# Optimization experiments

Hardware: AMD Instinct MI355X
Metric: run time of the kernel (lower is better)

Reference implementation:

```python
import jax, jax.numpy as jnp
import numpy as np

B, S, H = 2, 2048, 1024
G, HEADS = 4, 16
HPG = HEADS // G          # heads per group = 4
HD = H // HEADS           # head_dim = 64
DG = H // G               # per-group proj dim = 256
SCALE = 1.0 / np.sqrt(HD)


def setup_inputs() -> dict:
    key = jax.random.key(0)
    ks = jax.random.split(key, 6)
    w = 0.02
    return {
        "hidden_states": jax.random.normal(ks[0], (B, S, H), dtype=jnp.float32),
        "Wq": jax.random.normal(ks[1], (G, DG, H), dtype=jnp.float32) * w,
        "bq": jnp.zeros((G, DG), dtype=jnp.float32),
        "Wk": jax.random.normal(ks[2], (G, DG, H), dtype=jnp.float32) * w,
        "bk": jnp.zeros((G, DG), dtype=jnp.float32),
        "Wv": jax.random.normal(ks[3], (G, DG, H), dtype=jnp.float32) * w,
        "bv": jnp.zeros((G, DG), dtype=jnp.float32),
        "Wo": jax.random.normal(ks[4], (H, H), dtype=jnp.float32) * w,
        "bo": jnp.zeros((H,), dtype=jnp.float32),
    }


def _proj_split(x, W, b):
    # x: [B,S,H], W: [G,DG,H], b: [G,DG] -> [B,G,HPG,S,HD]
    y = jnp.einsum("bsh,gdh->bgsd", x, W) + b[None, :, None, :]
    y = y.reshape(x.shape[0], G, x.shape[1], HPG, HD)
    return jnp.transpose(y, (0, 1, 3, 2, 4))


def reference(hidden_states, Wq, bq, Wk, bk, Wv, bv, Wo, bo):
    q = _proj_split(hidden_states, Wq, bq)  # [B,G,HPG,S,HD]
    k = _proj_split(hidden_states, Wk, bk)
    v = _proj_split(hidden_states, Wv, bv)
    scores = jnp.einsum("bghqd,bghkd->bghqk", q, k) * SCALE
    attn = jax.nn.softmax(scores.astype(jnp.float32), axis=-1).astype(v.dtype)
    ctx = jnp.einsum("bghqk,bghkd->bghqd", attn, v)  # [B,G,HPG,S,HD]
    # merge: heads ordered group-major, matching torch cat over group dim
    ctx = jnp.transpose(ctx, (0, 3, 1, 2, 4)).reshape(hidden_states.shape[0], hidden_states.shape[1], H)
    return jnp.einsum("bsh,oh->bso", ctx, Wo) + bo
```

## Files before the change

### kernel.cpp

```cpp
#include <hip/hip_runtime.h>

typedef __bf16 bf16x8 __attribute__((ext_vector_type(8)));
typedef __bf16 bf16x4 __attribute__((ext_vector_type(4)));
typedef short short4v __attribute__((ext_vector_type(4)));
typedef float f32x4 __attribute__((ext_vector_type(4)));

#define LOG2E 1.4426950408889634f

static __device__ __forceinline__ unsigned short f2bf(float f) {
  union { float f; unsigned int u; } c; c.f = f;
  return (unsigned short)((c.u + 0x7fffu + ((c.u >> 16) & 1u)) >> 16);
}

static __device__ __forceinline__ void gload16(const void* g, void* l) {
  __builtin_amdgcn_global_load_lds(
      (const __attribute__((address_space(1))) void*)g,
      (__attribute__((address_space(3))) void*)l, 16, 0, 0);
}

static __device__ __forceinline__ float expfast(float x) {
#if __has_builtin(__builtin_amdgcn_exp2f)
  return __builtin_amdgcn_exp2f(x * LOG2E);
#else
  return exp2f(x * LOG2E);
#endif
}

#if __has_builtin(__builtin_amdgcn_mfma_f32_16x16x16bf16_1k)
#define MFMA16_FALLBACK 0
static __device__ __forceinline__ f32x4 mfma16(bf16x4 a, bf16x4 b, f32x4 c) {
  return __builtin_amdgcn_mfma_f32_16x16x16bf16_1k(
      __builtin_bit_cast(short4v, a), __builtin_bit_cast(short4v, b), c, 0, 0, 0);
}
#else
#define MFMA16_FALLBACK 1
static __device__ __forceinline__ f32x4 mfma16(bf16x4 a, bf16x4 b, f32x4 c) {
  f32x4 d;
  asm("s_nop 1\n\tv_mfma_f32_16x16x16_bf16 %0, %1, %2, %3"
      : "=v"(d) : "v"(a), "v"(b), "v"(c));
  return d;
}
#endif

__global__ void cvt_kernel(const float* __restrict__ in,
                           unsigned short* __restrict__ out, int n4) {
  int i = blockIdx.x * 256 + threadIdx.x;
  if (i < n4) {
    float4 f = ((const float4*)in)[i];
    ushort4 o;
    o.x = f2bf(f.x); o.y = f2bf(f.y); o.z = f2bf(f.z); o.w = f2bf(f.w);
    ((ushort4*)out)[i] = o;
  }
}

__launch_bounds__(256, 2)
__global__ void qkv_gemm(const unsigned short* __restrict__ xb,
                         const unsigned short* __restrict__ wq,
                         const unsigned short* __restrict__ wk,
                         const unsigned short* __restrict__ wv,
                         const float* __restrict__ bq,
                         const float* __restrict__ bk,
                         const float* __restrict__ bv,
                         unsigned short* __restrict__ Qo,
                         unsigned short* __restrict__ Ko,
                         unsigned short* __restrict__ Vo) {
  __shared__ unsigned short As[128 * 32];
  __shared__ unsigned short Bs[128 * 32];
  const int m0 = blockIdx.x * 128;
  const int n0g = blockIdx.y * 128;
  const int qkv = n0g >> 10;
  const int n0 = n0g & 1023;
  const unsigned short* W = (qkv == 0) ? wq : ((qkv == 1) ? wk : wv);
  const float* bias = (qkv == 0) ? bq : ((qkv == 1) ? bk : bv);
  unsigned short* OUT = (qkv == 0) ? Qo : ((qkv == 1) ? Ko : Vo);

  const int tid = threadIdx.x;
  const int lane = tid & 63;
  const int wid = tid >> 6;
  const int wm = (wid >> 1) * 64;
  const int wn = (wid & 1) * 64;
  const int lm = lane & 15;
  const int lq = lane >> 4;

  const int c0 = tid, c1 = 256 + tid;
  const int ar0 = c0 >> 2, aj0 = c0 & 3;
  const int ar1 = c1 >> 2, aj1 = c1 & 3;

  f32x4 acc[4][4] = {};

  for (int kk = 0; kk < 1024; kk += 32) {
    gload16(xb + (size_t)(m0 + ar0) * 1024 + kk + aj0 * 8, As + c0 * 8);
    gload16(xb + (size_t)(m0 + ar1) * 1024 + kk + aj1 * 8, As + c1 * 8);
    gload16(W + (size_t)(n0 + ar0) * 1024 + kk + aj0 * 8, Bs + c0 * 8);
    gload16(W + (size_t)(n0 + ar1) * 1024 + kk + aj1 * 8, Bs + c1 * 8);
    __syncthreads();
    bf16x8 af[4], bff[4];
#pragma unroll
    for (int mt = 0; mt < 4; ++mt)
      af[mt] = *(const bf16x8*)(As + (wm + mt * 16 + lm) * 32 + lq * 8);
#pragma unroll
    for (int nt = 0; nt < 4; ++nt)
      bff[nt] = *(const bf16x8*)(Bs + (wn + nt * 16 + lm) * 32 + lq * 8);
#pragma unroll
    for (int mt = 0; mt < 4; ++mt)
#pragma unroll
      for (int nt = 0; nt < 4; ++nt)
        acc[mt][nt] = __builtin_amdgcn_mfma_f32_16x16x32_bf16(
            af[mt], bff[nt], acc[mt][nt], 0, 0, 0);
    __syncthreads();
  }

  const float scale = (qkv == 0) ? 0.125f : 1.0f;
#pragma unroll
  for (int nt = 0; nt < 4; ++nt) {
    const int col = n0 + wn + nt * 16 + lm;
    const int g = col >> 8, d = col & 255;
    const int hpg = d >> 6, hd = d & 63;
    const float bb = bias[col];
#pragma unroll
    for (int mt = 0; mt < 4; ++mt) {
#pragma unroll
      for (int r = 0; r < 4; ++r) {
        const int srow = m0 + wm + mt * 16 + lq * 4 + r;
        const int bidx = srow >> 11, s = srow & 2047;
        const int head = (bidx * 4 + g) * 4 + hpg;
        OUT[(size_t)head * 131072 + (size_t)s * 64 + hd] =
            f2bf((acc[mt][nt][r] + bb) * scale);
      }
    }
  }
}

__global__ void vtrans(const unsigned short* __restrict__ V,
                       unsigned short* __restrict__ VT) {
  __shared__ unsigned short tile[64][65];
  const int head = blockIdx.y;
  const int kv0 = blockIdx.x * 64;
  const unsigned short* src = V + (size_t)head * 131072 + (size_t)kv0 * 64;
  unsigned short* dst = VT + (size_t)head * 131072 + kv0;
  const int tid = threadIdx.x;
#pragma unroll
  for (int i = 0; i < 16; ++i) {
    int e = i * 256 + tid;
    int r = e >> 6, c = e & 63;
    tile[r][c] = src[r * 64 + c];
  }
  __syncthreads();
#pragma unroll
  for (int i = 0; i < 16; ++i) {
    int e = i * 256 + tid;
    int r = e >> 6, c = e & 63;
    dst[(size_t)r * 2048 + c] = tile[c][r];
  }
}

static __device__ __forceinline__ void stage_kv(
    const unsigned short* Kh, const unsigned short* Vh, int kv0,
    unsigned short* ksl, unsigned short* vsl, int tid) {
#pragma unroll
  for (int t = 0; t < 4; ++t) {
    int i = t * 256 + tid;
    int slab = i >> 9, kv = (i >> 2) & 127, tp = i & 3;
    int tc = tp ^ ((kv >> 1) & 3);
    gload16(Kh + (size_t)(kv0 + kv) * 64 + slab * 32 + tc * 8, ksl + (size_t)i * 8);
  }
#pragma unroll
  for (int t = 0; t < 4; ++t) {
    int i = t * 256 + tid;
    int hd = i >> 4, tp = i & 15;
    int tc = tp ^ ((hd >> 1) & 7);
    gload16(Vh + (size_t)hd * 2048 + kv0 + tc * 8, vsl + (size_t)i * 8);
  }
}

__launch_bounds__(256, 2)
__global__ void attn_kernel(const unsigned short* __restrict__ Q,
                            const unsigned short* __restrict__ K,
                            const unsigned short* __restrict__ VT,
                            unsigned short* __restrict__ ctx) {
  __shared__ unsigned short Ks[2][8192];
  __shared__ unsigned short Vs[2][8192];

  const int head = blockIdx.y;
  const int q0 = blockIdx.x * 128;
  const int b = head >> 4;
  const int colbase = (head & 15) * 64;

  const unsigned short* Kh = K + (size_t)head * 131072;
  const unsigned short* Vh = VT + (size_t)head * 131072;

  const int tid = threadIdx.x;
  const int lane = tid & 63;
  const int w = tid >> 6;
  const int lm = lane & 15;
  const int quad = lane >> 4;

  bf16x8 qf[2][2];
#pragma unroll
  for (int nt = 0; nt < 2; ++nt) {
    const size_t qrow = (size_t)(q0 + w * 32 + nt * 16 + lm);
#pragma unroll
    for (int c = 0; c < 2; ++c)
      qf[c][nt] = *(const bf16x8*)(Q + (size_t)head * 131072 + qrow * 64 +
                                   c * 32 + quad * 8);
  }

  stage_kv(Kh, Vh, 0, Ks[0], Vs[0], tid);
  __syncthreads();

  float psum[2] = {0.f, 0.f};
  f32x4 oacc[4][2] = {};
  const int kchunk = (quad ^ ((lm >> 1) & 3)) * 8;

  for (int it = 0; it < 16; ++it) {
    const int buf = it & 1;
    if (it < 15)
      stage_kv(Kh, Vh, (it + 1) * 128, Ks[buf ^ 1], Vs[buf ^ 1], tid);

    const unsigned short* kb = Ks[buf];
    const unsigned short* vb = Vs[buf];

#pragma unroll
    for (int mt = 0; mt < 8; ++mt) {
      f32x4 s0 = {}, s1 = {};
#pragma unroll
      for (int c = 0; c < 2; ++c) {
        bf16x8 kf = *(const bf16x8*)(kb + c * 4096 + (mt * 16 + lm) * 32 + kchunk);
        s0 = __builtin_amdgcn_mfma_f32_16x16x32_bf16(kf, qf[c][0], s0, 0, 0, 0);
        s1 = __builtin_amdgcn_mfma_f32_16x16x32_bf16(kf, qf[c][1], s1, 0, 0, 0);
      }
      bf16x4 pf[2];
#pragma unroll
      for (int nt = 0; nt < 2; ++nt) {
        const f32x4 s = nt ? s1 : s0;
        float e0 = expfast(s[0]), e1 = expfast(s[1]);
        float e2 = expfast(s[2]), e3 = expfast(s[3]);
        psum[nt] += (e0 + e1) + (e2 + e3);
        bf16x4 t;
        t[0] = (__bf16)e0; t[1] = (__bf16)e1; t[2] = (__bf16)e2; t[3] = (__bf16)e3;
        pf[nt] = t;
      }
#pragma unroll
      for (int hm = 0; hm < 4; ++hm) {
        bf16x4 vf = *(const bf16x4*)(vb + (hm * 16 + lm) * 128 +
                                     (((mt * 4 + quad) ^ (lm & 14)) * 4));
        oacc[hm][0] = mfma16(vf, pf[0], oacc[hm][0]);
        oacc[hm][1] = mfma16(vf, pf[1], oacc[hm][1]);
      }
    }
    __syncthreads();
  }

#if MFMA16_FALLBACK
  asm volatile("s_nop 7\n\ts_nop 7");
#endif
#pragma unroll
  for (int nt = 0; nt < 2; ++nt) {
    float p = psum[nt];
    p += __shfl_xor(p, 16, 64);
    p += __shfl_xor(p, 32, 64);
    const float inv = 1.0f / p;
    const size_t row = (size_t)(b * 2048 + q0 + w * 32 + nt * 16 + lm);
#pragma unroll
    for (int hm = 0; hm < 4; ++hm) {
      ushort4 o;
      o.x = f2bf(oacc[hm][nt][0] * inv);
      o.y = f2bf(oacc[hm][nt][1] * inv);
      o.z = f2bf(oacc[hm][nt][2] * inv);
      o.w = f2bf(oacc[hm][nt][3] * inv);
      *(ushort4*)(ctx + row * 1024 + colbase + hm * 16 + quad * 4) = o;
    }
  }
}

__launch_bounds__(256, 2)
__global__ void out_gemm(const unsigned short* __restrict__ A,
                         const unsigned short* __restrict__ Wb,
                         const float* __restrict__ bo,
                         float* __restrict__ out) {
  __shared__ unsigned short As[128 * 32];
  __shared__ unsigned short Bs[128 * 32];
  const int m0 = blockIdx.x * 128;
  const int n0 = blockIdx.y * 128;

  const int tid = threadIdx.x;
  const int lane = tid & 63;
  const int wid = tid >> 6;
  const int wm = (wid >> 1) * 64;
  const int wn = (wid & 1) * 64;
  const int lm = lane & 15;
  const int lq = lane >> 4;

  const int c0 = tid, c1 = 256 + tid;
  const int ar0 = c0 >> 2, aj0 = c0 & 3;
  const int ar1 = c1 >> 2, aj1 = c1 & 3;

  f32x4 acc[4][4] = {};

  for (int kk = 0; kk < 1024; kk += 32) {
    gload16(A + (size_t)(m0 + ar0) * 1024 + kk + aj0 * 8, As + c0 * 8);
    gload16(A + (size_t)(m0 + ar1) * 1024 + kk + aj1 * 8, As + c1 * 8);
    gload16(Wb + (size_t)(n0 + ar0) * 1024 + kk + aj0 * 8, Bs + c0 * 8);
    gload16(Wb + (size_t)(n0 + ar1) * 1024 + kk + aj1 * 8, Bs + c1 * 8);
    __syncthreads();
    bf16x8 af[4], bff[4];
#pragma unroll
    for (int mt = 0; mt < 4; ++mt)
      af[mt] = *(const bf16x8*)(As + (wm + mt * 16 + lm) * 32 + lq * 8);
#pragma unroll
    for (int nt = 0; nt < 4; ++nt)
      bff[nt] = *(const bf16x8*)(Bs + (wn + nt * 16 + lm) * 32 + lq * 8);
#pragma unroll
    for (int mt = 0; mt < 4; ++mt)
#pragma unroll
      for (int nt = 0; nt < 4; ++nt)
        acc[mt][nt] = __builtin_amdgcn_mfma_f32_16x16x32_bf16(
            af[mt], bff[nt], acc[mt][nt], 0, 0, 0);
    __syncthreads();
  }

#pragma unroll
  for (int nt = 0; nt < 4; ++nt) {
    const int col = n0 + wn + nt * 16 + lm;
    const float bb = bo[col];
#pragma unroll
    for (int mt = 0; mt < 4; ++mt) {
#pragma unroll
      for (int r = 0; r < 4; ++r) {
        const int row = m0 + wm + mt * 16 + lq * 4 + r;
        out[(size_t)row * 1024 + col] = acc[mt][nt][r] + bb;
      }
    }
  }
}

extern "C" void kernel_launch(void* const* d_in, const int* in_sizes, int n_in,
                              void* d_out, int out_size, void* d_ws, size_t ws_size,
                              hipStream_t stream) {
  const float* x  = (const float*)d_in[0];
  const float* Wq = (const float*)d_in[1];
  const float* bq = (const float*)d_in[2];
  const float* Wk = (const float*)d_in[3];
  const float* bk = (const float*)d_in[4];
  const float* Wv = (const float*)d_in[5];
  const float* bv = (const float*)d_in[6];
  const float* Wo = (const float*)d_in[7];
  const float* bo = (const float*)d_in[8];
  float* out = (float*)d_out;

  char* ws = (char*)d_ws;
  unsigned short* xb  = (unsigned short*)(ws + 0);
  unsigned short* wqb = (unsigned short*)(ws + 8388608);
  unsigned short* wkb = (unsigned short*)(ws + 10485760);
  unsigned short* wvb = (unsigned short*)(ws + 12582912);
  unsigned short* wob = (unsigned short*)(ws + 14680064);
  unsigned short* Qb  = (unsigned short*)(ws + 16777216);
  unsigned short* Kb  = (unsigned short*)(ws + 25165824);
  unsigned short* Vb  = (unsigned short*)(ws + 33554432);
  unsigned short* VTb = (unsigned short*)(ws + 41943040);
  unsigned short* ctxb= (unsigned short*)(ws + 50331648);
  if (ws_size < 58720256) return;

  cvt_kernel<<<4096, 256, 0, stream>>>(x,  xb,  1048576);
  cvt_kernel<<<1024, 256, 0, stream>>>(Wq, wqb, 262144);
  cvt_kernel<<<1024, 256, 0, stream>>>(Wk, wkb, 262144);
  cvt_kernel<<<1024, 256, 0, stream>>>(Wv, wvb, 262144);
  cvt_kernel<<<1024, 256, 0, stream>>>(Wo, wob, 262144);

  qkv_gemm<<<dim3(32, 24), 256, 0, stream>>>(xb, wqb, wkb, wvb, bq, bk, bv,
                                             Qb, Kb, Vb);
  vtrans<<<dim3(32, 32), 256, 0, stream>>>(Vb, VTb);
  attn_kernel<<<dim3(16, 32), 256, 0, stream>>>(Qb, Kb, VTb, ctxb);
  out_gemm<<<dim3(32, 8), 256, 0, stream>>>(ctxb, wob, bo, out);
}
```

Measured before the change: 205.9 us.

## Fuse conversions, write V transposed from QKV GEMM, vectorize epilogue stores

Merges the five fp32-to-bf16 conversion launches into one kernel. The QKV GEMM now swaps its operands per output so Q/K epilogues and the out-projection store contiguous 4-element vectors. The V projection writes directly in transposed layout, which removes the separate vtrans kernel and its extra round trip through memory. Cost in exchange: branching on which operand is which inside the GEMM, and strided ushort4 stores for V^T.

```diff
diff --git a/kernel.cpp b/kernel.cpp
--- a/kernel.cpp
+++ b/kernel.cpp
@@ -42,15 +42,26 @@
 }
 #endif
 
-__global__ void cvt_kernel(const float* __restrict__ in,
-                           unsigned short* __restrict__ out, int n4) {
+__global__ void cvt_all(const float* __restrict__ x,
+                        const float* __restrict__ Wq,
+                        const float* __restrict__ Wk,
+                        const float* __restrict__ Wv,
+                        const float* __restrict__ Wo,
+                        ushort4* __restrict__ dst) {
   int i = blockIdx.x * 256 + threadIdx.x;
-  if (i < n4) {
-    float4 f = ((const float4*)in)[i];
-    ushort4 o;
-    o.x = f2bf(f.x); o.y = f2bf(f.y); o.z = f2bf(f.z); o.w = f2bf(f.w);
-    ((ushort4*)out)[i] = o;
-  }
+  const float* src;
+  int off;
+  if (i < 1048576) {
+    src = x; off = i;
+  } else {
+    int t = (i - 1048576) >> 18;
+    off = (i - 1048576) & 262143;
+    src = (t == 0) ? Wq : (t == 1) ? Wk : (t == 2) ? Wv : Wo;
+  }
+  float4 f = ((const float4*)src)[off];
+  ushort4 o;
+  o.x = f2bf(f.x); o.y = f2bf(f.y); o.z = f2bf(f.z); o.w = f2bf(f.w);
+  dst[i] = o;
 }
 
 __launch_bounds__(256, 2)
@@ -63,16 +74,20 @@
                          const float* __restrict__ bv,
                          unsigned short* __restrict__ Qo,
                          unsigned short* __restrict__ Ko,
-                         unsigned short* __restrict__ Vo) {
+                         unsigned short* __restrict__ VTo) {
   __shared__ unsigned short As[128 * 32];
   __shared__ unsigned short Bs[128 * 32];
-  const int m0 = blockIdx.x * 128;
+  const int s0 = blockIdx.x * 128;
   const int n0g = blockIdx.y * 128;
   const int qkv = n0g >> 10;
-  const int n0 = n0g & 1023;
+  const int d0 = n0g & 1023;
   const unsigned short* W = (qkv == 0) ? wq : ((qkv == 1) ? wk : wv);
   const float* bias = (qkv == 0) ? bq : ((qkv == 1) ? bk : bv);
-  unsigned short* OUT = (qkv == 0) ? Qo : ((qkv == 1) ? Ko : Vo);
+
+  const unsigned short* Aptr; const unsigned short* Bptr;
+  int Aoff, Boff;
+  if (qkv < 2) { Aptr = W;  Aoff = d0; Bptr = xb; Boff = s0; }
+  else         { Aptr = xb; Aoff = s0; Bptr = W;  Boff = d0; }
 
   const int tid = threadIdx.x;
   const int lane = tid & 63;
@@ -80,7 +95,7 @@
   const int wm = (wid >> 1) * 64;
   const int wn = (wid & 1) * 64;
   const int lm = lane & 15;
-  const int lq = lane >> 4;
+  const int quad = lane >> 4;
 
   const int c0 = tid, c1 = 256 + tid;
   const int ar0 = c0 >> 2, aj0 = c0 & 3;
@@ -89,18 +104,18 @@
   f32x4 acc[4][4] = {};
 
   for (int kk = 0; kk < 1024; kk += 32) {
-    gload16(xb + (size_t)(m0 + ar0) * 1024 + kk + aj0 * 8, As + c0 * 8);
-    gload16(xb + (size_t)(m0 + ar1) * 1024 + kk + aj1 * 8, As + c1 * 8);
-    gload16(W + (size_t)(n0 + ar0) * 1024 + kk + aj0 * 8, Bs + c0 * 8);
-    gload16(W + (size_t)(n0 + ar1) * 1024 + kk + aj1 * 8, Bs + c1 * 8);
+    gload16(Aptr + (size_t)(Aoff + ar0) * 1024 + kk + aj0 * 8, As + c0 * 8);
+    gload16(Aptr + (size_t)(Aoff + ar1) * 1024 + kk + aj1 * 8, As + c1 * 8);
+    gload16(Bptr + (size_t)(Boff + ar0) * 1024 + kk + aj0 * 8, Bs + c0 * 8);
+    gload16(Bptr + (size_t)(Boff + ar1) * 1024 + kk + aj1 * 8, Bs + c1 * 8);
     __syncthreads();
     bf16x8 af[4], bff[4];
 #pragma unroll
     for (int mt = 0; mt < 4; ++mt)
-      af[mt] = *(const bf16x8*)(As + (wm + mt * 16 + lm) * 32 + lq * 8);
+      af[mt] = *(const bf16x8*)(As + (wm + mt * 16 + lm) * 32 + quad * 8);
 #pragma unroll
     for (int nt = 0; nt < 4; ++nt)
-      bff[nt] = *(const bf16x8*)(Bs + (wn + nt * 16 + lm) * 32 + lq * 8);
+      bff[nt] = *(const bf16x8*)(Bs + (wn + nt * 16 + lm) * 32 + quad * 8);
 #pragma unroll
     for (int mt = 0; mt < 4; ++mt)
 #pragma unroll
@@ -110,47 +125,46 @@
     __syncthreads();
   }
 
-  const float scale = (qkv == 0) ? 0.125f : 1.0f;
-#pragma unroll
-  for (int nt = 0; nt < 4; ++nt) {
-    const int col = n0 + wn + nt * 16 + lm;
-    const int g = col >> 8, d = col & 255;
-    const int hpg = d >> 6, hd = d & 63;
-    const float bb = bias[col];
+  if (qkv < 2) {
+    unsigned short* OUT = (qkv == 0) ? Qo : Ko;
+    const float scale = (qkv == 0) ? 0.125f : 1.0f;
 #pragma unroll
     for (int mt = 0; mt < 4; ++mt) {
-#pragma unroll
-      for (int r = 0; r < 4; ++r) {
-        const int srow = m0 + wm + mt * 16 + lq * 4 + r;
+      const int d = d0 + wm + mt * 16 + quad * 4;
+      const int g = d >> 8, hpg = (d >> 6) & 3, hd = d & 63;
+      const float4 bb = *(const float4*)(bias + d);
+#pragma unroll
+      for (int nt = 0; nt < 4; ++nt) {
+        const int srow = s0 + wn + nt * 16 + lm;
         const int bidx = srow >> 11, s = srow & 2047;
         const int head = (bidx * 4 + g) * 4 + hpg;
-        OUT[(size_t)head * 131072 + (size_t)s * 64 + hd] =
-            f2bf((acc[mt][nt][r] + bb) * scale);
-      }
-    }
-  }
-}
-
-__global__ void vtrans(const unsigned short* __restrict__ V,
-                       unsigned short* __restrict__ VT) {
-  __shared__ unsigned short tile[64][65];
-  const int head = blockIdx.y;
-  const int kv0 = blockIdx.x * 64;
-  const unsigned short* src = V + (size_t)head * 131072 + (size_t)kv0 * 64;
-  unsigned short* dst = VT + (size_t)head * 131072 + kv0;
-  const int tid = threadIdx.x;
-#pragma unroll
-  for (int i = 0; i < 16; ++i) {
-    int e = i * 256 + tid;
-    int r = e >> 6, c = e & 63;
-    tile[r][c] = src[r * 64 + c];
-  }
-  __syncthreads();
-#pragma unroll
-  for (int i = 0; i < 16; ++i) {
-    int e = i * 256 + tid;
-    int r = e >> 6, c = e & 63;
-    dst[(size_t)r * 2048 + c] = tile[c][r];
+        ushort4 o;
+        o.x = f2bf((acc[mt][nt][0] + bb.x) * scale);
+        o.y = f2bf((acc[mt][nt][1] + bb.y) * scale);
+        o.z = f2bf((acc[mt][nt][2] + bb.z) * scale);
+        o.w = f2bf((acc[mt][nt][3] + bb.w) * scale);
+        *(ushort4*)(OUT + (size_t)head * 131072 + (size_t)s * 64 + hd) = o;
+      }
+    }
+  } else {
+#pragma unroll
+    for (int nt = 0; nt < 4; ++nt) {
+      const int d = d0 + wn + nt * 16 + lm;
+      const int g = d >> 8, hpg = (d >> 6) & 3, hd = d & 63;
+      const float bb = bias[d];
+#pragma unroll
+      for (int mt = 0; mt < 4; ++mt) {
+        const int sbase = s0 + wm + mt * 16 + quad * 4;
+        const int bidx = sbase >> 11, s = sbase & 2047;
+        const int head = (bidx * 4 + g) * 4 + hpg;
+        ushort4 o;
+        o.x = f2bf(acc[mt][nt][0] + bb);
+        o.y = f2bf(acc[mt][nt][1] + bb);
+        o.z = f2bf(acc[mt][nt][2] + bb);
+        o.w = f2bf(acc[mt][nt][3] + bb);
+        *(ushort4*)(VTo + (size_t)head * 131072 + (size_t)hd * 2048 + s) = o;
+      }
+    }
   }
 }
 
@@ -280,8 +294,8 @@
                          float* __restrict__ out) {
   __shared__ unsigned short As[128 * 32];
   __shared__ unsigned short Bs[128 * 32];
-  const int m0 = blockIdx.x * 128;
-  const int n0 = blockIdx.y * 128;
+  const int s0 = blockIdx.x * 128;
+  const int o0 = blockIdx.y * 128;
 
   const int tid = threadIdx.x;
   const int lane = tid & 63;
@@ -289,7 +303,7 @@
   const int wm = (wid >> 1) * 64;
   const int wn = (wid & 1) * 64;
   const int lm = lane & 15;
-  const int lq = lane >> 4;
+  const int quad = lane >> 4;
 
   const int c0 = tid, c1 = 256 + tid;
   const int ar0 = c0 >> 2, aj0 = c0 & 3;
@@ -298,18 +312,18 @@
   f32x4 acc[4][4] = {};
 
   for (int kk = 0; kk < 1024; kk += 32) {
-    gload16(A + (size_t)(m0 + ar0) * 1024 + kk + aj0 * 8, As + c0 * 8);
-    gload16(A + (size_t)(m0 + ar1) * 1024 + kk + aj1 * 8, As + c1 * 8);
-    gload16(Wb + (size_t)(n0 + ar0) * 1024 + kk + aj0 * 8, Bs + c0 * 8);
-    gload16(Wb + (size_t)(n0 + ar1) * 1024 + kk + aj1 * 8, Bs + c1 * 8);
+    gload16(Wb + (size_t)(o0 + ar0) * 1024 + kk + aj0 * 8, As + c0 * 8);
+    gload16(Wb + (size_t)(o0 + ar1) * 1024 + kk + aj1 * 8, As + c1 * 8);
+    gload16(A + (size_t)(s0 + ar0) * 1024 + kk + aj0 * 8, Bs + c0 * 8);
+    gload16(A + (size_t)(s0 + ar1) * 1024 + kk + aj1 * 8, Bs + c1 * 8);
     __syncthreads();
     bf16x8 af[4], bff[4];
 #pragma unroll
     for (int mt = 0; mt < 4; ++mt)
-      af[mt] = *(const bf16x8*)(As + (wm + mt * 16 + lm) * 32 + lq * 8);
+      af[mt] = *(const bf16x8*)(As + (wm + mt * 16 + lm) * 32 + quad * 8);
 #pragma unroll
     for (int nt = 0; nt < 4; ++nt)
-      bff[nt] = *(const bf16x8*)(Bs + (wn + nt * 16 + lm) * 32 + lq * 8);
+      bff[nt] = *(const bf16x8*)(Bs + (wn + nt * 16 + lm) * 32 + quad * 8);
 #pragma unroll
     for (int mt = 0; mt < 4; ++mt)
 #pragma unroll
@@ -320,16 +334,18 @@
   }
 
 #pragma unroll
-  for (int nt = 0; nt < 4; ++nt) {
-    const int col = n0 + wn + nt * 16 + lm;
-    const float bb = bo[col];
-#pragma unroll
-    for (int mt = 0; mt < 4; ++mt) {
-#pragma unroll
-      for (int r = 0; r < 4; ++r) {
-        const int row = m0 + wm + mt * 16 + lq * 4 + r;
-        out[(size_t)row * 1024 + col] = acc[mt][nt][r] + bb;
-      }
+  for (int mt = 0; mt < 4; ++mt) {
+    const int o = o0 + wm + mt * 16 + quad * 4;
+    const float4 bb = *(const float4*)(bo + o);
+#pragma unroll
+    for (int nt = 0; nt < 4; ++nt) {
+      const int s = s0 + wn + nt * 16 + lm;
+      float4 v;
+      v.x = acc[mt][nt][0] + bb.x;
+      v.y = acc[mt][nt][1] + bb.y;
+      v.z = acc[mt][nt][2] + bb.z;
+      v.w = acc[mt][nt][3] + bb.w;
+      *(float4*)(out + (size_t)s * 1024 + o) = v;
     }
   }
 }
@@ -356,20 +372,13 @@
   unsigned short* wob = (unsigned short*)(ws + 14680064);
   unsigned short* Qb  = (unsigned short*)(ws + 16777216);
   unsigned short* Kb  = (unsigned short*)(ws + 25165824);
-  unsigned short* Vb  = (unsigned short*)(ws + 33554432);
-  unsigned short* VTb = (unsigned short*)(ws + 41943040);
-  unsigned short* ctxb= (unsigned short*)(ws + 50331648);
-  if (ws_size < 58720256) return;
-
-  cvt_kernel<<<4096, 256, 0, stream>>>(x,  xb,  1048576);
-  cvt_kernel<<<1024, 256, 0, stream>>>(Wq, wqb, 262144);
-  cvt_kernel<<<1024, 256, 0, stream>>>(Wk, wkb, 262144);
-  cvt_kernel<<<1024, 256, 0, stream>>>(Wv, wvb, 262144);
-  cvt_kernel<<<1024, 256, 0, stream>>>(Wo, wob, 262144);
-
+  unsigned short* VTb = (unsigned short*)(ws + 33554432);
+  unsigned short* ctxb= (unsigned short*)(ws + 41943040);
+  if (ws_size < 50331648) return;
+
+  cvt_all<<<8192, 256, 0, stream>>>(x, Wq, Wk, Wv, Wo, (ushort4*)ws);
   qkv_gemm<<<dim3(32, 24), 256, 0, stream>>>(xb, wqb, wkb, wvb, bq, bk, bv,
-                                             Qb, Kb, Vb);
-  vtrans<<<dim3(32, 32), 256, 0, stream>>>(Vb, VTb);
+                                             Qb, Kb, VTb);
   attn_kernel<<<dim3(16, 32), 256, 0, stream>>>(Qb, Kb, VTb, ctxb);
   out_gemm<<<dim3(32, 8), 256, 0, stream>>>(ctxb, wob, bo, out);
 }
```

Result: faster. 198.5 us (-3.6%).
